# Performance work log

Hardware: AMD Instinct MI355X
Metric: run time of the kernel (lower is better)

## Reference

```python
import jax, jax.numpy as jnp
import numpy as np

H = 50  # hidden size hard-coded in the module

def _lstm_cell(x, h, c, Wih, Whh, bih, bhh):
    # torch.nn.LSTMCell: gates ordered i, f, g, o
    g = x @ Wih.T + bih + h @ Whh.T + bhh  # [B, 4H]
    i, f, gg, o = jnp.split(g, 4, axis=-1)
    c2 = jax.nn.sigmoid(f) * c + jax.nn.sigmoid(i) * jnp.tanh(gg)
    h2 = jax.nn.sigmoid(o) * jnp.tanh(c2)
    return h2, c2

def setup_inputs() -> dict:
    key = jax.random.key(0)
    ks = jax.random.split(key, 10)
    B, T = 2048, 1024
    s1 = 1.0 / np.sqrt(H)
    u = lambda k, shp: jax.random.uniform(k, shp, jnp.float32, -s1, s1)
    return {
        "x": jax.random.normal(ks[0], (B, T), jnp.float32),
        "W_ih1": u(ks[1], (4 * H, 1)),
        "W_hh1": u(ks[2], (4 * H, H)),
        "b_ih1": u(ks[3], (4 * H,)),
        "b_hh1": u(ks[4], (4 * H,)),
        "W_ih2": u(ks[5], (4 * H, H)),
        "W_hh2": u(ks[6], (4 * H, H)),
        "b_ih2": u(ks[7], (4 * H,)),
        "b_hh2": u(ks[8], (4 * H,)),
        "W_lin": u(ks[9], (1, H)),
        "b_lin": jnp.zeros((1,), jnp.float32),
    }

def reference(x, W_ih1, W_hh1, b_ih1, b_hh1, W_ih2, W_hh2, b_ih2, b_hh2, W_lin, b_lin):
    # future=0 path; dropout is identity in eval mode.
    B = x.shape[0]
    xT = x.T[:, :, None]  # [T, B, 1]
    z = jnp.zeros((B, H), x.dtype)

    def step(carry, xt):
        h1, c1, h2, c2 = carry
        h1, c1 = _lstm_cell(xt, h1, c1, W_ih1, W_hh1, b_ih1, b_hh1)
        h2, c2 = _lstm_cell(h1, h2, c2, W_ih2, W_hh2, b_ih2, b_hh2)
        return (h1, c1, h2, c2), None

    (h1, c1, h2, c2), _ = jax.lax.scan(step, (z, z, z, z), xT)
    # outputs[:, -1] == linear(h_t2) at the final timestep
    out = h2 @ W_lin.T + b_lin  # [B, 1]
    return out[:, 0]
```

## Files before the change

kernel.cpp:

```cpp
#include <hip/hip_runtime.h>


#define TT 1024
#define HH 50
#define NB 8
#define NT 832
#define NTILE 13
#define VSZ 2112

typedef _Float16 f16x8 __attribute__((ext_vector_type(8)));
typedef unsigned short ushort8 __attribute__((ext_vector_type(8)));
typedef float f32x4 __attribute__((ext_vector_type(4)));

#define NLOG2E  -1.4426950408889634f
#define N2LOG2E -2.8853900817779268f

__device__ __forceinline__ float fast_rcp(float x) { return __builtin_amdgcn_rcpf(x); }
__device__ __forceinline__ float exp2f_hw(float x) { return __builtin_amdgcn_exp2f(x); }
__device__ __forceinline__ unsigned short f16bits(float f) {
    _Float16 h = (_Float16)f;
    return __builtin_bit_cast(unsigned short, h);
}
__device__ __forceinline__ float f16tof(unsigned short b) {
    return (float)__builtin_bit_cast(_Float16, b);
}
__device__ __forceinline__ float dpp_merge(float a, float b) {
    return __int_as_float(__builtin_amdgcn_update_dpp(
        __float_as_int(a), __float_as_int(b), 0x118, 0xF, 0xC, false));
}

__device__ __forceinline__ int vidx(int k, int n) {
    return ((k >> 3) << 7) + n * 8 + (k & 7);
}

__global__ __launch_bounds__(NT) void lstm_kernel(
    const float* __restrict__ x,
    const float* __restrict__ W_ih1, const float* __restrict__ W_hh1,
    const float* __restrict__ b_ih1, const float* __restrict__ b_hh1,
    const float* __restrict__ W_ih2, const float* __restrict__ W_hh2,
    const float* __restrict__ b_ih2, const float* __restrict__ b_hh2,
    const float* __restrict__ W_lin, const float* __restrict__ b_lin,
    float* __restrict__ out)
{
    __shared__ float xs[TT * NB];
    __shared__ __attribute__((aligned(16))) unsigned short v[2][VSZ];

    const int tid  = threadIdx.x;
    const int w    = tid >> 6;
    const int L    = tid & 63;
    const int quad = L >> 4;
    const int n15  = L & 15;
    const int b0g  = blockIdx.x * NB;

    const int  m     = w;
    const int  u     = m * 4 + quad;
    const bool low   = (n15 < NB);
    const bool updOK = (u < HH);
    const bool ldB   = low;
    const bool xw    = (w == 12) && (L >= 32) && (L < 32 + NB);
    const int  xb    = L - 32;
    const int hslot = updOK ? (low ? vidx(1 + u, n15) : vidx(51 + u, n15 - NB))
                            : (2048 + L);

    for (int i = tid; i < 2 * VSZ; i += NT) ((unsigned short*)v)[i] = 0;
    for (int i = tid; i < NB * TT; i += NT) {
        int b = i >> 10, t = i & 1023;
        xs[t * NB + b] = x[(size_t)b0g * TT + i];
    }

    f16x8 a1[2], a2[4];
    f32x4 bias1 = {0.f, 0.f, 0.f, 0.f}, bias2 = {0.f, 0.f, 0.f, 0.f};
    float c = 0.f;

    {
        const int arow = m * 16 + n15;
        const bool av = (arow < 200);
        const int r = av ? ((arow & 3) * 50 + (arow >> 2)) : 0;
        const float sc = ((arow & 3) == 2) ? N2LOG2E : NLOG2E;
        #pragma unroll
        for (int kt = 0; kt < 2; ++kt) {
            ushort8 th;
            #pragma unroll
            for (int j = 0; j < 8; ++j) {
                int k = kt * 32 + quad * 8 + j;
                float wv = 0.f;
                if (av) { if (k == 0) wv = W_ih1[r]; else if (k <= 50) wv = W_hh1[r * 50 + k - 1]; }
                th[j] = f16bits(wv * sc);
            }
            a1[kt] = __builtin_bit_cast(f16x8, th);
        }
        #pragma unroll
        for (int kt = 0; kt < 4; ++kt) {
            ushort8 th;
            #pragma unroll
            for (int j = 0; j < 8; ++j) {
                int k = kt * 32 + quad * 8 + j;
                float wv = 0.f;
                if (av) {
                    if (k >= 1 && k <= 50) wv = W_ih2[r * 50 + k - 1];
                    else if (k >= 51 && k <= 100) wv = W_hh2[r * 50 + k - 51];
                }
                th[j] = f16bits(wv * sc);
            }
            a2[kt] = __builtin_bit_cast(f16x8, th);
        }
        #pragma unroll
        for (int reg = 0; reg < 4; ++reg) {
            int crow = m * 16 + quad * 4 + reg;
            if (crow < 200) {
                int rr = (crow & 3) * 50 + (crow >> 2);
                float s2 = ((crow & 3) == 2) ? N2LOG2E : NLOG2E;
                bias1[reg] = s2 * (b_ih1[rr] + b_hh1[rr]);
                bias2[reg] = s2 * (b_ih2[rr] + b_hh2[rr]);
            }
        }
    }

    __syncthreads();
    if (tid < NB) v[0][vidx(0, tid)] = f16bits(xs[0 * NB + tid]);
    __syncthreads();

    f16x8 bfr[4];
    #pragma unroll
    for (int kt = 0; kt < 4; ++kt)
        bfr[kt] = __builtin_bit_cast(f16x8, ushort8{0,0,0,0,0,0,0,0});

    auto body = [&](int t, const unsigned short* vr, unsigned short* vw,
                    bool doL1, bool doL2, bool masked) {
        if (ldB) {
            #pragma unroll
            for (int kt = 0; kt < 4; ++kt)
                bfr[kt] = ((const f16x8*)vr)[kt * 64 + L];
        }
        f32x4 aM1 = bias1, aM2 = bias2;
        if (doL1) {
            #pragma unroll
            for (int kt = 0; kt < 2; ++kt)
                aM1 = __builtin_amdgcn_mfma_f32_16x16x32_f16(a1[kt], bfr[kt], aM1, 0, 0, 0);
        }
        if (doL2) {
            #pragma unroll
            for (int kt = 0; kt < 4; ++kt)
                aM2 = __builtin_amdgcn_mfma_f32_16x16x32_f16(a2[kt], bfr[kt], aM2, 0, 0, 0);
        }
        f32x4 g;
        #pragma unroll
        for (int r = 0; r < 4; ++r) g[r] = dpp_merge(aM1[r], aM2[r]);

        if (!masked || (updOK && low)) {
            float ei = exp2f_hw(g[0]);
            float ef = exp2f_hw(g[1]);
            float eg = exp2f_hw(g[2]);
            float eo = exp2f_hw(g[3]);
            float p  = (1.0f + ei) * (1.0f + eg);
            float q  = (1.0f - eg) * (1.0f + ef);
            float cn = fmaf(c, p, q) * fast_rcp(p * (1.0f + ef));
            c = cn;
            float ecn = exp2f_hw(cn * N2LOG2E);
            float h = (1.0f - ecn) * fast_rcp((1.0f + eo) * (1.0f + ecn));
            vw[hslot] = f16bits(h);
        }
        if (xw && t + 1 < TT) vw[vidx(0, xb)] = f16bits(xs[(t + 1) * NB + xb]);
        __syncthreads();
    };

    body(0, v[0], v[1], true, false, true);
    body(1, v[1], v[0], true, true, false);
    for (int t = 2; t < TT; t += 2) {
        body(t,     v[0], v[1], true, true, false);
        body(t + 1, v[1], v[0], true, true, false);
    }
    body(TT, v[0], v[1], false, true, false);

    if (tid < NB) {
        float s = b_lin[0];
        #pragma unroll
        for (int uu = 0; uu < HH; ++uu)
            s += W_lin[uu] * f16tof(v[1][vidx(51 + uu, tid)]);
        out[b0g + tid] = s;
    }
}

extern "C" void kernel_launch(void* const* d_in, const int* in_sizes, int n_in,
                              void* d_out, int out_size, void* d_ws, size_t ws_size,
                              hipStream_t stream) {
    const float* x     = (const float*)d_in[0];
    const float* W_ih1 = (const float*)d_in[1];
    const float* W_hh1 = (const float*)d_in[2];
    const float* b_ih1 = (const float*)d_in[3];
    const float* b_hh1 = (const float*)d_in[4];
    const float* W_ih2 = (const float*)d_in[5];
    const float* W_hh2 = (const float*)d_in[6];
    const float* b_ih2 = (const float*)d_in[7];
    const float* b_hh2 = (const float*)d_in[8];
    const float* W_lin = (const float*)d_in[9];
    const float* b_lin = (const float*)d_in[10];
    float* out = (float*)d_out;

    const int Btot = in_sizes[0] / TT;
    const int nblocks = Btot / NB;

    lstm_kernel<<<nblocks, NT, 0, stream>>>(
        x, W_ih1, W_hh1, b_ih1, b_hh1, W_ih2, W_hh2, b_ih2, b_hh2,
        W_lin, b_lin, out);
}
```

Measured before the change: 534.1 us.

## Shrink LSTM block to 8 waves with two MFMA tiles per wave

The block drops from 13 waves (832 threads) to 8 waves (512 threads). Waves 0-4 now each handle two 16-row gate tiles and waves 5-7 handle one, with per-tile weights, biases and cell state kept in registers. The aim is a cheaper per-timestep __syncthreads across fewer waves and room for two blocks per CU (launch_bounds 512,2). In exchange the per-wave serial work is uneven (some waves do double MFMA and activation math), which lengthens the critical path of each step, and register pressure rises.

```diff
diff --git a/kernel.cpp b/kernel.cpp
--- a/kernel.cpp
+++ b/kernel.cpp
@@ -4,8 +4,7 @@
 #define TT 1024
 #define HH 50
 #define NB 8
-#define NT 832
-#define NTILE 13
+#define NT 512
 #define VSZ 2112
 
 typedef _Float16 f16x8 __attribute__((ext_vector_type(8)));
@@ -33,7 +32,7 @@
     return ((k >> 3) << 7) + n * 8 + (k & 7);
 }
 
-__global__ __launch_bounds__(NT) void lstm_kernel(
+__global__ __launch_bounds__(NT, 2) void lstm_kernel(
     const float* __restrict__ x,
     const float* __restrict__ W_ih1, const float* __restrict__ W_hh1,
     const float* __restrict__ b_ih1, const float* __restrict__ b_hh1,
@@ -52,15 +51,21 @@
     const int n15  = L & 15;
     const int b0g  = blockIdx.x * NB;
 
-    const int  m     = w;
-    const int  u     = m * 4 + quad;
-    const bool low   = (n15 < NB);
-    const bool updOK = (u < HH);
-    const bool ldB   = low;
-    const bool xw    = (w == 12) && (L >= 32) && (L < 32 + NB);
-    const int  xb    = L - 32;
-    const int hslot = updOK ? (low ? vidx(1 + u, n15) : vidx(51 + u, n15 - NB))
+    const int  np   = (w < 5) ? 2 : 1;
+    const bool low  = (n15 < NB);
+    const bool ldB  = low;
+    const bool xw   = (w == 7) && (L < NB);
+
+    int  mA[2];  mA[0] = w;  mA[1] = w + 8;
+    int  hslot[2];
+    bool updOK[2];
+    #pragma unroll
+    for (int p = 0; p < 2; ++p) {
+        int u = mA[p] * 4 + quad;
+        updOK[p] = (u < HH);
+        hslot[p] = updOK[p] ? (low ? vidx(1 + u, n15) : vidx(51 + u, n15 - NB))
                             : (2048 + L);
+    }
 
     for (int i = tid; i < 2 * VSZ; i += NT) ((unsigned short*)v)[i] = 0;
     for (int i = tid; i < NB * TT; i += NT) {
@@ -68,13 +73,16 @@
         xs[t * NB + b] = x[(size_t)b0g * TT + i];
     }
 
-    f16x8 a1[2], a2[4];
-    f32x4 bias1 = {0.f, 0.f, 0.f, 0.f}, bias2 = {0.f, 0.f, 0.f, 0.f};
-    float c = 0.f;
-
-    {
+    f16x8 a1[2][2], a2[2][4];
+    f32x4 bias1[2], bias2[2];
+    float c[2] = {0.f, 0.f};
+
+    #pragma unroll
+    for (int p = 0; p < 2; ++p) {
+        const int m = mA[p];
+        const bool pv = (p < np);
         const int arow = m * 16 + n15;
-        const bool av = (arow < 200);
+        const bool av = pv && (arow < 200);
         const int r = av ? ((arow & 3) * 50 + (arow >> 2)) : 0;
         const float sc = ((arow & 3) == 2) ? N2LOG2E : NLOG2E;
         #pragma unroll
@@ -87,7 +95,7 @@
                 if (av) { if (k == 0) wv = W_ih1[r]; else if (k <= 50) wv = W_hh1[r * 50 + k - 1]; }
                 th[j] = f16bits(wv * sc);
             }
-            a1[kt] = __builtin_bit_cast(f16x8, th);
+            a1[p][kt] = __builtin_bit_cast(f16x8, th);
         }
         #pragma unroll
         for (int kt = 0; kt < 4; ++kt) {
@@ -102,18 +110,20 @@
                 }
                 th[j] = f16bits(wv * sc);
             }
-            a2[kt] = __builtin_bit_cast(f16x8, th);
-        }
+            a2[p][kt] = __builtin_bit_cast(f16x8, th);
+        }
+        f32x4 bb1 = {0.f,0.f,0.f,0.f}, bb2 = {0.f,0.f,0.f,0.f};
         #pragma unroll
         for (int reg = 0; reg < 4; ++reg) {
             int crow = m * 16 + quad * 4 + reg;
-            if (crow < 200) {
+            if (pv && crow < 200) {
                 int rr = (crow & 3) * 50 + (crow >> 2);
                 float s2 = ((crow & 3) == 2) ? N2LOG2E : NLOG2E;
-                bias1[reg] = s2 * (b_ih1[rr] + b_hh1[rr]);
-                bias2[reg] = s2 * (b_ih2[rr] + b_hh2[rr]);
-            }
-        }
+                bb1[reg] = s2 * (b_ih1[rr] + b_hh1[rr]);
+                bb2[reg] = s2 * (b_ih2[rr] + b_hh2[rr]);
+            }
+        }
+        bias1[p] = bb1; bias2[p] = bb2;
     }
 
     __syncthreads();
@@ -132,35 +142,43 @@
             for (int kt = 0; kt < 4; ++kt)
                 bfr[kt] = ((const f16x8*)vr)[kt * 64 + L];
         }
-        f32x4 aM1 = bias1, aM2 = bias2;
+        f32x4 aM1[2], aM2[2];
+        #pragma unroll
+        for (int p = 0; p < 2; ++p) { aM1[p] = bias1[p]; aM2[p] = bias2[p]; }
         if (doL1) {
             #pragma unroll
             for (int kt = 0; kt < 2; ++kt)
-                aM1 = __builtin_amdgcn_mfma_f32_16x16x32_f16(a1[kt], bfr[kt], aM1, 0, 0, 0);
+                #pragma unroll
+                for (int p = 0; p < 2; ++p) if (p < np)
+                    aM1[p] = __builtin_amdgcn_mfma_f32_16x16x32_f16(a1[p][kt], bfr[kt], aM1[p], 0, 0, 0);
         }
         if (doL2) {
             #pragma unroll
             for (int kt = 0; kt < 4; ++kt)
-                aM2 = __builtin_amdgcn_mfma_f32_16x16x32_f16(a2[kt], bfr[kt], aM2, 0, 0, 0);
-        }
-        f32x4 g;
-        #pragma unroll
-        for (int r = 0; r < 4; ++r) g[r] = dpp_merge(aM1[r], aM2[r]);
-
-        if (!masked || (updOK && low)) {
-            float ei = exp2f_hw(g[0]);
-            float ef = exp2f_hw(g[1]);
-            float eg = exp2f_hw(g[2]);
-            float eo = exp2f_hw(g[3]);
-            float p  = (1.0f + ei) * (1.0f + eg);
-            float q  = (1.0f - eg) * (1.0f + ef);
-            float cn = fmaf(c, p, q) * fast_rcp(p * (1.0f + ef));
-            c = cn;
-            float ecn = exp2f_hw(cn * N2LOG2E);
-            float h = (1.0f - ecn) * fast_rcp((1.0f + eo) * (1.0f + ecn));
-            vw[hslot] = f16bits(h);
-        }
-        if (xw && t + 1 < TT) vw[vidx(0, xb)] = f16bits(xs[(t + 1) * NB + xb]);
+                #pragma unroll
+                for (int p = 0; p < 2; ++p) if (p < np)
+                    aM2[p] = __builtin_amdgcn_mfma_f32_16x16x32_f16(a2[p][kt], bfr[kt], aM2[p], 0, 0, 0);
+        }
+        #pragma unroll
+        for (int p = 0; p < 2; ++p) if (p < np) {
+            f32x4 g;
+            #pragma unroll
+            for (int r = 0; r < 4; ++r) g[r] = dpp_merge(aM1[p][r], aM2[p][r]);
+            if (!masked || (updOK[p] && low)) {
+                float ei = exp2f_hw(g[0]);
+                float ef = exp2f_hw(g[1]);
+                float eg = exp2f_hw(g[2]);
+                float eo = exp2f_hw(g[3]);
+                float pp = (1.0f + ei) * (1.0f + eg);
+                float qq = (1.0f - eg) * (1.0f + ef);
+                float cn = fmaf(c[p], pp, qq) * fast_rcp(pp * (1.0f + ef));
+                c[p] = cn;
+                float ecn = exp2f_hw(cn * N2LOG2E);
+                float h = (1.0f - ecn) * fast_rcp((1.0f + eo) * (1.0f + ecn));
+                vw[hslot[p]] = f16bits(h);
+            }
+        }
+        if (xw && t + 1 < TT) vw[vidx(0, L)] = f16bits(xs[(t + 1) * NB + L]);
         __syncthreads();
     };
 
```

Result: slower. 609.6 us (+14.1%).
